# Kernel tuning notes

Hardware: AMD Instinct MI355X
Metric: run time of the kernel (lower is better)

Reference implementation:

```python
import jax, jax.numpy as jnp
import numpy as np

B, T, U, D, V = 8, 256, 64, 512, 1024

def setup_inputs() -> dict:
    key = jax.random.key(0)
    k1, k2, k3, k4, k5, k6 = jax.random.split(key, 6)
    source_encodings = jax.random.normal(k1, (B, T, D), dtype=jnp.float32)
    target_encodings = jax.random.normal(k2, (B, U, D), dtype=jnp.float32)
    source_lengths = jax.random.randint(k3, (B,), 1, T + 1, dtype=jnp.int32)
    target_lengths = jax.random.randint(k4, (B,), 1, U + 1, dtype=jnp.int32)
    # nn.Linear(D, V): weight (V, D), bias (V,)
    bound = 1.0 / np.sqrt(D)
    W = jax.random.uniform(k5, (V, D), minval=-bound, maxval=bound, dtype=jnp.float32)
    b = jax.random.uniform(k6, (V,), minval=-bound, maxval=bound, dtype=jnp.float32)
    return {"source_encodings": source_encodings, "source_lengths": source_lengths,
            "target_encodings": target_encodings, "target_lengths": target_lengths,
            "W": W, "b": b}

def reference(source_encodings, source_lengths, target_encodings, target_lengths, W, b):
    # (B,T,1,D) + (B,1,U,D) -> (B,T,U,D); dropout p=0.0 is identity (eval/no-op)
    joint = source_encodings[:, :, None, :] + target_encodings[:, None, :, :]
    act = jax.nn.relu(joint)
    # Linear: act @ W^T + b -> (B,T,U,V)
    out = jnp.einsum('btud,vd->btuv', act, W) + b
    return out, source_lengths, target_lengths
```

## Files before the change

kernel.cpp:

```cpp
#include <hip/hip_runtime.h>
#include <hip/hip_bf16.h>

#define B_ 8
#define T_ 256
#define U_ 64
#define D_ 512
#define V_ 1024
#define M_ (B_*T_*U_)

typedef __attribute__((ext_vector_type(8))) short bf16x8;
typedef __attribute__((ext_vector_type(4))) float f32x4;

__device__ __forceinline__ void gld_lds16(const void* g, void* l) {
    __builtin_amdgcn_global_load_lds(
        (const __attribute__((address_space(1))) void*)g,
        (__attribute__((address_space(3))) void*)l, 16, 0, 0);
}

__global__ void prep_kernel(const float* __restrict__ W,
                            const int* __restrict__ slen, const int* __restrict__ tlen,
                            __hip_bfloat16* __restrict__ Wt,
                            float* __restrict__ lenout) {
    int t = blockIdx.x * 256 + threadIdx.x;
    int n  = t >> 6;
    int k8 = t & 63;
    const float4* p = (const float4*)(W + (size_t)n * D_ + k8 * 8);
    float4 a = p[0], c = p[1];
    union { __hip_bfloat16 h[8]; bf16x8 v; } u;
    u.h[0] = __float2bfloat16(a.x); u.h[1] = __float2bfloat16(a.y);
    u.h[2] = __float2bfloat16(a.z); u.h[3] = __float2bfloat16(a.w);
    u.h[4] = __float2bfloat16(c.x); u.h[5] = __float2bfloat16(c.y);
    u.h[6] = __float2bfloat16(c.z); u.h[7] = __float2bfloat16(c.w);
    int j = n >> 7, nl = n & 127;
    *(bf16x8*)(Wt + ((size_t)(j * 64 + k8) * 128 + nl) * 8) = u.v;
    if (blockIdx.x == 0 && threadIdx.x < 8) {
        lenout[threadIdx.x]     = (float)slen[threadIdx.x];
        lenout[8 + threadIdx.x] = (float)tlen[threadIdx.x];
    }
}

__device__ __forceinline__ bf16x8 pack_relu8(float4 s0, float4 s1, float4 g0, float4 g1) {
    union { __hip_bfloat16 h[8]; bf16x8 v; } u;
    u.h[0] = __float2bfloat16(fmaxf(s0.x + g0.x, 0.f));
    u.h[1] = __float2bfloat16(fmaxf(s0.y + g0.y, 0.f));
    u.h[2] = __float2bfloat16(fmaxf(s0.z + g0.z, 0.f));
    u.h[3] = __float2bfloat16(fmaxf(s0.w + g0.w, 0.f));
    u.h[4] = __float2bfloat16(fmaxf(s1.x + g1.x, 0.f));
    u.h[5] = __float2bfloat16(fmaxf(s1.y + g1.y, 0.f));
    u.h[6] = __float2bfloat16(fmaxf(s1.z + g1.z, 0.f));
    u.h[7] = __float2bfloat16(fmaxf(s1.w + g1.w, 0.f));
    return u.v;
}

__global__ __launch_bounds__(256) void joiner_gemm(
    const float* __restrict__ src, const float* __restrict__ tgt,
    const __hip_bfloat16* __restrict__ Wt, const float* __restrict__ bias,
    float* __restrict__ out) {
    __shared__ __hip_bfloat16 Bs[2 * 8192];

    const int tid = threadIdx.x;
    const int bx  = blockIdx.x;
    const int bid = (bx & 7) * 1024 + (bx >> 3);
    const int tileN = bid & 7;
    const int tileM = bid >> 3;
    const int m_base = tileM * 128;
    const int b  = m_base >> 14;
    const int t0 = (m_base & 16383) >> 6;

    const int wid = tid >> 6, lane = tid & 63;
    const int lrow = lane & 15, lk = lane >> 4;

    const float* srcP  = src + (size_t)(b * T_ + t0 + (wid >> 1)) * D_;
    const float* tgtP0 = tgt + (size_t)(b * U_ + (wid & 1) * 32 + lrow) * D_;
    const float* tgtP1 = tgtP0 + 16 * D_;

    const __hip_bfloat16* WtT = Wt + (size_t)tileN * 64 * 128 * 8;
    const __hip_bfloat16* BsR = Bs + ((size_t)lk * 128 + lrow) * 8;

    f32x4 acc[2][8] = {};

    #pragma unroll
    for (int i = 0; i < 4; ++i) {
        const int wi = wid * 4 + i;
        gld_lds16(WtT + ((size_t)wi * 64 + lane) * 8, (void*)(Bs + wi * 512));
    }
    __syncthreads();

    #pragma unroll
    for (int kk = 0; kk < 8; ++kk) {
        const int cur = kk & 1;
        if (kk < 7) {
            const __hip_bfloat16* g = WtT + (size_t)(kk + 1) * 8192;
            __hip_bfloat16* dst = Bs + (cur ^ 1) * 8192;
            #pragma unroll
            for (int i = 0; i < 4; ++i) {
                const int wi = wid * 4 + i;
                gld_lds16(g + ((size_t)wi * 64 + lane) * 8, (void*)(dst + wi * 512));
            }
        }
        const int kbase = kk * 64 + lk * 8;
        #pragma unroll
        for (int ks = 0; ks < 2; ++ks) {
            const int ko = kbase + ks * 32;
            float4 s0 = *(const float4*)(srcP + ko);
            float4 s1 = *(const float4*)(srcP + ko + 4);
            float4 ga = *(const float4*)(tgtP0 + ko);
            float4 gb = *(const float4*)(tgtP0 + ko + 4);
            float4 gc = *(const float4*)(tgtP1 + ko);
            float4 gd = *(const float4*)(tgtP1 + ko + 4);
            bf16x8 af0 = pack_relu8(s0, s1, ga, gb);
            bf16x8 af1 = pack_relu8(s0, s1, gc, gd);
            const __hip_bfloat16* br = BsR + cur * 8192 + ks * 4096;
            bf16x8 bfr[8];
            #pragma unroll
            for (int j = 0; j < 8; ++j)
                bfr[j] = *(const bf16x8*)(br + j * 128);
            #pragma unroll
            for (int j = 0; j < 8; ++j) {
                acc[0][j] = __builtin_amdgcn_mfma_f32_16x16x32_bf16(af0, bfr[j], acc[0][j], 0, 0, 0);
                acc[1][j] = __builtin_amdgcn_mfma_f32_16x16x32_bf16(af1, bfr[j], acc[1][j], 0, 0, 0);
            }
        }
        if (kk != 7) __syncthreads();
    }

    const int n0 = tileN * 128;
    float bv[8];
    #pragma unroll
    for (int j = 0; j < 8; ++j) bv[j] = bias[n0 + j * 16 + lrow];
    const int mrow0 = m_base + wid * 32 + lk * 4;
    #pragma unroll
    for (int i = 0; i < 2; ++i) {
        #pragma unroll
        for (int r = 0; r < 4; ++r) {
            float* orow = out + (size_t)(mrow0 + i * 16 + r) * V_;
            #pragma unroll
            for (int j = 0; j < 8; ++j)
                orow[n0 + j * 16 + lrow] = acc[i][j][r] + bv[j];
        }
    }
}

extern "C" void kernel_launch(void* const* d_in, const int* in_sizes, int n_in,
                              void* d_out, int out_size, void* d_ws, size_t ws_size,
                              hipStream_t stream) {
    const float* src  = (const float*)d_in[0];
    const int*   slen = (const int*)d_in[1];
    const float* tgt  = (const float*)d_in[2];
    const int*   tlen = (const int*)d_in[3];
    const float* W    = (const float*)d_in[4];
    const float* bias = (const float*)d_in[5];
    float* out = (float*)d_out;
    __hip_bfloat16* Wt = (__hip_bfloat16*)d_ws;

    prep_kernel<<<256, 256, 0, stream>>>(W, slen, tlen, Wt, out + (size_t)M_ * V_);
    joiner_gemm<<<M_ / 128 * (V_ / 128), 256, 0, stream>>>(src, tgt, Wt, bias, out);
}
```

Measured before the change: 782.9 us.

## Stage target encodings through padded LDS and prefetch source slices

Target-encoding K-slices now go into a padded LDS tile using async global-to-LDS loads alongside the weight tile. Activation fragments are built from LDS instead of per-lane global float4 loads, and the next source slice is prefetched into registers. An occupancy hint of 3 blocks per CU is added. This is meant to cut redundant global/L2 traffic for target rows and hide load latency, at the cost of extra LDS, an additional barrier per K step, and possible register pressure from the launch bound.

```diff
diff --git a/kernel.cpp b/kernel.cpp
--- a/kernel.cpp
+++ b/kernel.cpp
@@ -52,11 +52,12 @@
     return u.v;
 }
 
-__global__ __launch_bounds__(256) void joiner_gemm(
+__global__ __launch_bounds__(256, 3) void joiner_gemm(
     const float* __restrict__ src, const float* __restrict__ tgt,
     const __hip_bfloat16* __restrict__ Wt, const float* __restrict__ bias,
     float* __restrict__ out) {
-    __shared__ __hip_bfloat16 Bs[2 * 8192];
+    __shared__ __align__(16) __hip_bfloat16 Bs[2 * 8192];
+    __shared__ __align__(16) float Tg[64 * 68];
 
     const int tid = threadIdx.x;
     const int bx  = blockIdx.x;
@@ -70,46 +71,69 @@
     const int wid = tid >> 6, lane = tid & 63;
     const int lrow = lane & 15, lk = lane >> 4;
 
-    const float* srcP  = src + (size_t)(b * T_ + t0 + (wid >> 1)) * D_;
-    const float* tgtP0 = tgt + (size_t)(b * U_ + (wid & 1) * 32 + lrow) * D_;
-    const float* tgtP1 = tgtP0 + 16 * D_;
+    const float* srcP = src + (size_t)(b * T_ + t0 + (wid >> 1)) * D_ + lk * 8;
+
+    const float* tgGp[5];
+    #pragma unroll
+    for (int i = 0; i < 5; ++i) {
+        const int c   = (i < 4) ? (wid * 4 + i) : 16;
+        const int s16 = c * 64 + lane;
+        const int u   = (s16 * 241) >> 12;
+        int slot = s16 - u * 17;
+        if (slot == 16) slot = 0;
+        tgGp[i] = tgt + (size_t)(b * U_ + u) * D_ + slot * 4;
+    }
 
     const __hip_bfloat16* WtT = Wt + (size_t)tileN * 64 * 128 * 8;
     const __hip_bfloat16* BsR = Bs + ((size_t)lk * 128 + lrow) * 8;
+    char* TgB = (char*)Tg;
+    const int wq = (wid & 1) * 32;
 
     f32x4 acc[2][8] = {};
+    bf16x8 afc[2][2];
+    float4 c0a, c0b, c1a, c1b, n0a, n0b, n1a, n1b;
 
-    #pragma unroll
-    for (int i = 0; i < 4; ++i) {
-        const int wi = wid * 4 + i;
-        gld_lds16(WtT + ((size_t)wi * 64 + lane) * 8, (void*)(Bs + wi * 512));
-    }
+#define STAGE(kkn, bbuf) { \
+    _Pragma("unroll") \
+    for (int i = 0; i < 4; ++i) { \
+        const int c = wid * 4 + i; \
+        gld_lds16(tgGp[i] + (kkn) * 64, (void*)(TgB + c * 1024)); \
+        gld_lds16(WtT + (size_t)(kkn) * 8192 + ((size_t)c * 64 + lane) * 8, \
+                  (void*)(Bs + (bbuf) * 8192 + c * 512)); \
+    } \
+    if (wid == 0) gld_lds16(tgGp[4] + (kkn) * 64, (void*)(TgB + 16 * 1024)); }
+
+    STAGE(0, 0)
+    c0a = *(const float4*)(srcP + 0);  c0b = *(const float4*)(srcP + 4);
+    c1a = *(const float4*)(srcP + 32); c1b = *(const float4*)(srcP + 36);
     __syncthreads();
 
     #pragma unroll
     for (int kk = 0; kk < 8; ++kk) {
         const int cur = kk & 1;
-        if (kk < 7) {
-            const __hip_bfloat16* g = WtT + (size_t)(kk + 1) * 8192;
-            __hip_bfloat16* dst = Bs + (cur ^ 1) * 8192;
-            #pragma unroll
-            for (int i = 0; i < 4; ++i) {
-                const int wi = wid * 4 + i;
-                gld_lds16(g + ((size_t)wi * 64 + lane) * 8, (void*)(dst + wi * 512));
+        #pragma unroll
+        for (int i = 0; i < 2; ++i) {
+            const int rowb = (wq + i * 16 + lrow) * 272;
+            {
+                const float4 ta = *(const float4*)(TgB + rowb + lk * 32);
+                const float4 tb = *(const float4*)(TgB + rowb + lk * 32 + 16);
+                afc[0][i] = pack_relu8(c0a, c0b, ta, tb);
+            }
+            {
+                const float4 ta = *(const float4*)(TgB + rowb + 128 + lk * 32);
+                const float4 tb = *(const float4*)(TgB + rowb + 128 + lk * 32 + 16);
+                afc[1][i] = pack_relu8(c1a, c1b, ta, tb);
             }
         }
-        const int kbase = kk * 64 + lk * 8;
+        __syncthreads();
+        if (kk < 7) {
+            const int ko = (kk + 1) * 64;
+            n0a = *(const float4*)(srcP + ko);      n0b = *(const float4*)(srcP + ko + 4);
+            n1a = *(const float4*)(srcP + ko + 32); n1b = *(const float4*)(srcP + ko + 36);
+            STAGE(kk + 1, cur ^ 1)
+        }
         #pragma unroll
         for (int ks = 0; ks < 2; ++ks) {
-            const int ko = kbase + ks * 32;
-            float4 s0 = *(const float4*)(srcP + ko);
-            float4 s1 = *(const float4*)(srcP + ko + 4);
-            float4 ga = *(const float4*)(tgtP0 + ko);
-            float4 gb = *(const float4*)(tgtP0 + ko + 4);
-            float4 gc = *(const float4*)(tgtP1 + ko);
-            float4 gd = *(const float4*)(tgtP1 + ko + 4);
-            bf16x8 af0 = pack_relu8(s0, s1, ga, gb);
-            bf16x8 af1 = pack_relu8(s0, s1, gc, gd);
             const __hip_bfloat16* br = BsR + cur * 8192 + ks * 4096;
             bf16x8 bfr[8];
             #pragma unroll
@@ -117,12 +141,16 @@
                 bfr[j] = *(const bf16x8*)(br + j * 128);
             #pragma unroll
             for (int j = 0; j < 8; ++j) {
-                acc[0][j] = __builtin_amdgcn_mfma_f32_16x16x32_bf16(af0, bfr[j], acc[0][j], 0, 0, 0);
-                acc[1][j] = __builtin_amdgcn_mfma_f32_16x16x32_bf16(af1, bfr[j], acc[1][j], 0, 0, 0);
+                acc[0][j] = __builtin_amdgcn_mfma_f32_16x16x32_bf16(afc[ks][0], bfr[j], acc[0][j], 0, 0, 0);
+                acc[1][j] = __builtin_amdgcn_mfma_f32_16x16x32_bf16(afc[ks][1], bfr[j], acc[1][j], 0, 0, 0);
             }
         }
-        if (kk != 7) __syncthreads();
+        if (kk < 7) {
+            c0a = n0a; c0b = n0b; c1a = n1a; c1b = n1b;
+            __syncthreads();
+        }
     }
+#undef STAGE
 
     const int n0 = tileN * 128;
     float bv[8];
```

Result: faster. 734.3 us (-6.2%).

## Enlarge GEMM tile to 128x256 with 8 waves and stage activations in LDS

Applied to the files above, without the earlier changes.

The joiner GEMM moves from 128x128 tiles with 4 waves to 128x256 tiles with 8 waves arranged 2x4, and the W layout is repacked to match. The fused add+ReLU activation tile is now built once per block in LDS and shared by the waves, so each wave no longer recomputes its own A fragments from global memory. Weight loads lose their double buffering and now use a single buffer with two barriers per k-step, which exposes load latency. The grid-swizzle block ordering is also dropped, which may hurt L2 reuse.

```diff
diff --git a/kernel.cpp b/kernel.cpp
--- a/kernel.cpp
+++ b/kernel.cpp
@@ -31,111 +31,110 @@
     u.h[2] = __float2bfloat16(a.z); u.h[3] = __float2bfloat16(a.w);
     u.h[4] = __float2bfloat16(c.x); u.h[5] = __float2bfloat16(c.y);
     u.h[6] = __float2bfloat16(c.z); u.h[7] = __float2bfloat16(c.w);
-    int j = n >> 7, nl = n & 127;
-    *(bf16x8*)(Wt + ((size_t)(j * 64 + k8) * 128 + nl) * 8) = u.v;
+    int j = n >> 8, nl = n & 255;
+    *(bf16x8*)(Wt + ((size_t)(j * 64 + k8) * 256 + nl) * 8) = u.v;
     if (blockIdx.x == 0 && threadIdx.x < 8) {
         lenout[threadIdx.x]     = (float)slen[threadIdx.x];
         lenout[8 + threadIdx.x] = (float)tlen[threadIdx.x];
     }
 }
 
-__device__ __forceinline__ bf16x8 pack_relu8(float4 s0, float4 s1, float4 g0, float4 g1) {
+__device__ __forceinline__ void relu_store8(__hip_bfloat16* dst,
+                                            float4 a, float4 a2, float4 b, float4 b2) {
     union { __hip_bfloat16 h[8]; bf16x8 v; } u;
-    u.h[0] = __float2bfloat16(fmaxf(s0.x + g0.x, 0.f));
-    u.h[1] = __float2bfloat16(fmaxf(s0.y + g0.y, 0.f));
-    u.h[2] = __float2bfloat16(fmaxf(s0.z + g0.z, 0.f));
-    u.h[3] = __float2bfloat16(fmaxf(s0.w + g0.w, 0.f));
-    u.h[4] = __float2bfloat16(fmaxf(s1.x + g1.x, 0.f));
-    u.h[5] = __float2bfloat16(fmaxf(s1.y + g1.y, 0.f));
-    u.h[6] = __float2bfloat16(fmaxf(s1.z + g1.z, 0.f));
-    u.h[7] = __float2bfloat16(fmaxf(s1.w + g1.w, 0.f));
-    return u.v;
+    u.h[0] = __float2bfloat16(fmaxf(a.x  + b.x,  0.f));
+    u.h[1] = __float2bfloat16(fmaxf(a.y  + b.y,  0.f));
+    u.h[2] = __float2bfloat16(fmaxf(a.z  + b.z,  0.f));
+    u.h[3] = __float2bfloat16(fmaxf(a.w  + b.w,  0.f));
+    u.h[4] = __float2bfloat16(fmaxf(a2.x + b2.x, 0.f));
+    u.h[5] = __float2bfloat16(fmaxf(a2.y + b2.y, 0.f));
+    u.h[6] = __float2bfloat16(fmaxf(a2.z + b2.z, 0.f));
+    u.h[7] = __float2bfloat16(fmaxf(a2.w + b2.w, 0.f));
+    *(bf16x8*)dst = u.v;
 }
 
-__global__ __launch_bounds__(256) void joiner_gemm(
+__global__ __launch_bounds__(512) void joiner_gemm(
     const float* __restrict__ src, const float* __restrict__ tgt,
     const __hip_bfloat16* __restrict__ Wt, const float* __restrict__ bias,
     float* __restrict__ out) {
-    __shared__ __hip_bfloat16 Bs[2 * 8192];
+    __shared__ __align__(16) __hip_bfloat16 As[128 * 72];
+    __shared__ __align__(16) __hip_bfloat16 Bs[8 * 256 * 8];
 
     const int tid = threadIdx.x;
     const int bx  = blockIdx.x;
-    const int bid = (bx & 7) * 1024 + (bx >> 3);
-    const int tileN = bid & 7;
-    const int tileM = bid >> 3;
+    const int tileN = bx & 3;
+    const int tileM = bx >> 2;
     const int m_base = tileM * 128;
     const int b  = m_base >> 14;
     const int t0 = (m_base & 16383) >> 6;
 
-    const int wid = tid >> 6, lane = tid & 63;
+    const int r0 = tid >> 3;
+    const int kc = (tid & 7) * 8;
+    const float* srcA = src + (size_t)(b * T_ + t0) * D_ + kc;
+    const float* srcB = srcA + D_;
+    const float* tgtA = tgt + (size_t)(b * U_ + r0) * D_ + kc;
+    __hip_bfloat16* As0 = As + r0 * 72 + kc;
+
+    const __hip_bfloat16* WtT = Wt + (size_t)tileN * 64 * 256 * 8;
+
+    const int wid  = tid >> 6, lane = tid & 63;
+    const int waveM = wid >> 2, waveN = wid & 3;
     const int lrow = lane & 15, lk = lane >> 4;
+    const __hip_bfloat16* AsW = As + (waveM * 64 + lrow) * 72 + lk * 8;
+    const __hip_bfloat16* BsW = Bs + ((size_t)lk * 256 + waveN * 64 + lrow) * 8;
 
-    const float* srcP  = src + (size_t)(b * T_ + t0 + (wid >> 1)) * D_;
-    const float* tgtP0 = tgt + (size_t)(b * U_ + (wid & 1) * 32 + lrow) * D_;
-    const float* tgtP1 = tgtP0 + 16 * D_;
+    f32x4 acc[4][4] = {};
 
-    const __hip_bfloat16* WtT = Wt + (size_t)tileN * 64 * 128 * 8;
-    const __hip_bfloat16* BsR = Bs + ((size_t)lk * 128 + lrow) * 8;
+    for (int kk = 0; kk < 8; ++kk) {
+        const __hip_bfloat16* gB = WtT + (size_t)kk * 16384;
+        #pragma unroll
+        for (int i = 0; i < 4; ++i) {
+            const int c = wid * 4 + i;
+            gld_lds16(gB + ((size_t)c * 64 + lane) * 8, (void*)(Bs + c * 512));
+        }
+        const int ko = kk * 64;
+        float4 s0  = *(const float4*)(srcA + ko);
+        float4 s0b = *(const float4*)(srcA + ko + 4);
+        float4 s1  = *(const float4*)(srcB + ko);
+        float4 s1b = *(const float4*)(srcB + ko + 4);
+        float4 g0  = *(const float4*)(tgtA + ko);
+        float4 g0b = *(const float4*)(tgtA + ko + 4);
+        relu_store8(As0,           s0, s0b, g0, g0b);
+        relu_store8(As0 + 64 * 72, s1, s1b, g0, g0b);
 
-    f32x4 acc[2][8] = {};
+        __syncthreads();
 
-    #pragma unroll
-    for (int i = 0; i < 4; ++i) {
-        const int wi = wid * 4 + i;
-        gld_lds16(WtT + ((size_t)wi * 64 + lane) * 8, (void*)(Bs + wi * 512));
-    }
-    __syncthreads();
-
-    #pragma unroll
-    for (int kk = 0; kk < 8; ++kk) {
-        const int cur = kk & 1;
-        if (kk < 7) {
-            const __hip_bfloat16* g = WtT + (size_t)(kk + 1) * 8192;
-            __hip_bfloat16* dst = Bs + (cur ^ 1) * 8192;
-            #pragma unroll
-            for (int i = 0; i < 4; ++i) {
-                const int wi = wid * 4 + i;
-                gld_lds16(g + ((size_t)wi * 64 + lane) * 8, (void*)(dst + wi * 512));
-            }
-        }
-        const int kbase = kk * 64 + lk * 8;
         #pragma unroll
         for (int ks = 0; ks < 2; ++ks) {
-            const int ko = kbase + ks * 32;
-            float4 s0 = *(const float4*)(srcP + ko);
-            float4 s1 = *(const float4*)(srcP + ko + 4);
-            float4 ga = *(const float4*)(tgtP0 + ko);
-            float4 gb = *(const float4*)(tgtP0 + ko + 4);
-            float4 gc = *(const float4*)(tgtP1 + ko);
-            float4 gd = *(const float4*)(tgtP1 + ko + 4);
-            bf16x8 af0 = pack_relu8(s0, s1, ga, gb);
-            bf16x8 af1 = pack_relu8(s0, s1, gc, gd);
-            const __hip_bfloat16* br = BsR + cur * 8192 + ks * 4096;
-            bf16x8 bfr[8];
+            bf16x8 af[4], bfr[4];
             #pragma unroll
-            for (int j = 0; j < 8; ++j)
-                bfr[j] = *(const bf16x8*)(br + j * 128);
+            for (int i = 0; i < 4; ++i)
+                af[i] = *(const bf16x8*)(AsW + i * 16 * 72 + ks * 32);
             #pragma unroll
-            for (int j = 0; j < 8; ++j) {
-                acc[0][j] = __builtin_amdgcn_mfma_f32_16x16x32_bf16(af0, bfr[j], acc[0][j], 0, 0, 0);
-                acc[1][j] = __builtin_amdgcn_mfma_f32_16x16x32_bf16(af1, bfr[j], acc[1][j], 0, 0, 0);
-            }
+            for (int j = 0; j < 4; ++j)
+                bfr[j] = *(const bf16x8*)(BsW + ks * 8192 + j * 128);
+            #pragma unroll
+            for (int i = 0; i < 4; ++i)
+                #pragma unroll
+                for (int j = 0; j < 4; ++j)
+                    acc[i][j] = __builtin_amdgcn_mfma_f32_16x16x32_bf16(
+                        af[i], bfr[j], acc[i][j], 0, 0, 0);
         }
         if (kk != 7) __syncthreads();
     }
 
-    const int n0 = tileN * 128;
-    float bv[8];
+    const int n0 = tileN * 256 + waveN * 64;
+    float bv[4];
     #pragma unroll
-    for (int j = 0; j < 8; ++j) bv[j] = bias[n0 + j * 16 + lrow];
-    const int mrow0 = m_base + wid * 32 + lk * 4;
+    for (int j = 0; j < 4; ++j) bv[j] = bias[n0 + j * 16 + lrow];
     #pragma unroll
-    for (int i = 0; i < 2; ++i) {
+    for (int i = 0; i < 4; ++i) {
+        const int mrow = m_base + waveM * 64 + i * 16 + lk * 4;
         #pragma unroll
         for (int r = 0; r < 4; ++r) {
-            float* orow = out + (size_t)(mrow0 + i * 16 + r) * V_;
+            float* orow = out + (size_t)(mrow + r) * V_;
             #pragma unroll
-            for (int j = 0; j < 8; ++j)
+            for (int j = 0; j < 4; ++j)
                 orow[n0 + j * 16 + lrow] = acc[i][j][r] + bv[j];
         }
     }
@@ -154,5 +153,5 @@
     __hip_bfloat16* Wt = (__hip_bfloat16*)d_ws;
 
     prep_kernel<<<256, 256, 0, stream>>>(W, slen, tlen, Wt, out + (size_t)M_ * V_);
-    joiner_gemm<<<M_ / 128 * (V_ / 128), 256, 0, stream>>>(src, tgt, Wt, bias, out);
+    joiner_gemm<<<(M_ / 128) * (V_ / 256), 512, 0, stream>>>(src, tgt, Wt, bias, out);
 }
```

Result: faster. 651.7 us (-16.8%).
